# Kernel tuning notes

Hardware: AMD Instinct MI355X
Metric: run time of the kernel (lower is better)

## Reference

```python
import jax, jax.numpy as jnp
import numpy as np

D_MODEL = 1024
NUM_HEADS = 16
D_K = D_MODEL // NUM_HEADS
B, S = 2, 2048


def setup_inputs() -> dict:
    key = jax.random.key(0)
    ks = jax.random.split(key, 9)
    scale = 1.0 / np.sqrt(D_MODEL)
    return {
        "hidden_states": jax.random.normal(ks[0], (B, S, D_MODEL), dtype=jnp.float32),
        "attention_mask": jnp.ones((B, S, S), dtype=jnp.int32),
        "Wq": jax.random.normal(ks[1], (D_MODEL, D_MODEL), dtype=jnp.float32) * scale,
        "bq": jnp.zeros((D_MODEL,), dtype=jnp.float32),
        "Wk": jax.random.normal(ks[2], (D_MODEL, D_MODEL), dtype=jnp.float32) * scale,
        "bk": jnp.zeros((D_MODEL,), dtype=jnp.float32),
        "Wv": jax.random.normal(ks[3], (D_MODEL, D_MODEL), dtype=jnp.float32) * scale,
        "bv": jnp.zeros((D_MODEL,), dtype=jnp.float32),
        "Wo": jax.random.normal(ks[4], (D_MODEL, D_MODEL), dtype=jnp.float32) * scale,
        "bo": jnp.zeros((D_MODEL,), dtype=jnp.float32),
    }


def reference(hidden_states, attention_mask, Wq, bq, Wk, bk, Wv, bv, Wo, bo):
    b, s, _ = hidden_states.shape
    # torch Linear: y = x @ W.T + b
    def proj(W, bias):
        y = jnp.einsum('bsd,ed->bse', hidden_states, W) + bias
        return y.reshape(b, s, NUM_HEADS, D_K).transpose(0, 2, 1, 3)  # [B,H,S,dk]
    q = proj(Wq, bq)
    k = proj(Wk, bk)
    v = proj(Wv, bv)
    scores = jnp.einsum('bnqd,bnkd->bnqk', q, k) / np.sqrt(D_K)
    mask = attention_mask[:, None, :, :]  # [B,1,S,S]
    scores = jnp.where(mask == 0, jnp.float32(-1e9), scores)
    attn = jax.nn.softmax(scores, axis=-1)  # dropout = identity (eval)
    ctx = jnp.einsum('bnqk,bnkd->bnqd', attn, v)
    ctx = ctx.transpose(0, 2, 1, 3).reshape(b, s, D_MODEL)
    return jnp.einsum('bsd,ed->bse', ctx, Wo) + bo
```

## Files before the change

### kernel.cpp

```cpp
#include <hip/hip_runtime.h>

typedef short short8 __attribute__((ext_vector_type(8)));
typedef float floatx4 __attribute__((ext_vector_type(4)));
typedef float floatx16 __attribute__((ext_vector_type(16)));
typedef unsigned short ushort4v __attribute__((ext_vector_type(4)));

#define DEV static __device__ __forceinline__

DEV unsigned short f2bf(float f) {
  unsigned int u = __builtin_bit_cast(unsigned int, f);
  u += 0x7fffu + ((u >> 16) & 1u);
  return (unsigned short)(u >> 16);
}

DEV unsigned int cvtpk(float a, float b) {
  unsigned int r;
  asm("v_cvt_pk_bf16_f32 %0, %1, %2" : "=v"(r) : "v"(a), "v"(b));
  return r;
}

DEV void gload16(const unsigned short* g, unsigned short* l) {
  __builtin_amdgcn_global_load_lds((__attribute__((address_space(1))) void*)g,
                                   (__attribute__((address_space(3))) void*)l,
                                   16, 0, 0);
}

__global__ void convert_kernel(const float* __restrict__ hs, const float* __restrict__ Wq,
                               const float* __restrict__ Wk, const float* __restrict__ Wv,
                               const float* __restrict__ Wo,
                               unsigned short* __restrict__ xbf, unsigned short* __restrict__ wqkv,
                               unsigned short* __restrict__ wobf) {
  size_t i4 = ((size_t)blockIdx.x * 256 + threadIdx.x) * 4;
  const float* src;
  unsigned short* dst;
  if (i4 < 4194304) {
    src = hs + i4; dst = xbf + i4;
  } else if (i4 < 7340032) {
    size_t o = i4 - 4194304;
    size_t lo = o & 1048575;
    src = (o < 1048576) ? (Wq + lo) : ((o < 2097152) ? (Wk + lo) : (Wv + lo));
    dst = wqkv + o;
  } else {
    size_t o = i4 - 7340032;
    src = Wo + o; dst = wobf + o;
  }
  float4 v = *(const float4*)src;
  ushort4v u;
  u.x = f2bf(v.x); u.y = f2bf(v.y); u.z = f2bf(v.z); u.w = f2bf(v.w);
  *(ushort4v*)dst = u;
}

__global__ void maskpack_kernel(const int* __restrict__ mask, unsigned long long* __restrict__ bits) {
  int w = blockIdx.x * 256 + threadIdx.x;
  const int4* p = (const int4*)(mask + (size_t)w * 64);
  unsigned long long r = 0ull;
#pragma unroll
  for (int j = 0; j < 16; ++j) {
    int4 m = p[j];
    r |= (unsigned long long)(m.x != 0) << (j * 4 + 0);
    r |= (unsigned long long)(m.y != 0) << (j * 4 + 1);
    r |= (unsigned long long)(m.z != 0) << (j * 4 + 2);
    r |= (unsigned long long)(m.w != 0) << (j * 4 + 3);
  }
  bits[w] = r;
}

__global__ void __launch_bounds__(256) qkv_gemm(
    const unsigned short* __restrict__ X, const unsigned short* __restrict__ W,
    const float* __restrict__ bq, const float* __restrict__ bk, const float* __restrict__ bv,
    unsigned short* __restrict__ Qb, unsigned short* __restrict__ Kb,
    unsigned short* __restrict__ Vt) {
  __shared__ __align__(16) unsigned short As[128 * 32];
  __shared__ __align__(16) unsigned short Bs[128 * 32];
  const int tid = threadIdx.x;
  const int lane = tid & 63, wv = tid >> 6;
  const int wm = wv >> 1, wn = wv & 1;
  const int quad = lane >> 4, l15 = lane & 15;
  const int mb = blockIdx.y, nb = blockIdx.x;
  const bool sw = (nb < 16);

  const unsigned short* ga = X + (size_t)(mb * 128 + (tid >> 2)) * 1024 + (tid & 3) * 8;
  const unsigned short* gb = W + (size_t)(nb * 128 + (tid >> 2)) * 1024 + (tid & 3) * 8;
  unsigned short* la1 = As + tid * 8;
  unsigned short* la2 = As + 2048 + tid * 8;
  unsigned short* lb1 = Bs + tid * 8;
  unsigned short* lb2 = Bs + 2048 + tid * 8;

  const int wx = sw ? wn : wm;
  const int ww = sw ? wm : wn;

  floatx4 acc[4][4] = {};
  for (int kt = 0; kt < 32; ++kt) {
    const int k0 = kt * 32;
    gload16(ga + k0, la1);
    gload16(ga + k0 + 65536, la2);
    gload16(gb + k0, lb1);
    gload16(gb + k0 + 65536, lb2);
    __syncthreads();
    short8 xa[4], wb[4];
#pragma unroll
    for (int i = 0; i < 4; ++i) {
      xa[i] = *(const short8*)&As[(wx * 64 + i * 16 + l15) * 32 + quad * 8];
      wb[i] = *(const short8*)&Bs[(ww * 64 + i * 16 + l15) * 32 + quad * 8];
    }
    if (sw) {
#pragma unroll
      for (int mt = 0; mt < 4; ++mt)
#pragma unroll
        for (int nt = 0; nt < 4; ++nt)
          acc[mt][nt] = __builtin_amdgcn_mfma_f32_16x16x32_bf16(wb[mt], xa[nt], acc[mt][nt], 0, 0, 0);
    } else {
#pragma unroll
      for (int mt = 0; mt < 4; ++mt)
#pragma unroll
        for (int nt = 0; nt < 4; ++nt)
          acc[mt][nt] = __builtin_amdgcn_mfma_f32_16x16x32_bf16(xa[mt], wb[nt], acc[mt][nt], 0, 0, 0);
    }
    __syncthreads();
  }

  if (sw) {
#pragma unroll
    for (int mt = 0; mt < 4; ++mt) {
      const int wc0 = nb * 128 + wm * 64 + mt * 16 + quad * 4;
      const int mat = wc0 >> 10;
      const int nl0 = wc0 & 1023;
      const int hh = nl0 >> 6, d0 = nl0 & 63;
      const float4 b4 = *(const float4*)((mat ? bk : bq) + nl0);
      unsigned short* dst = mat ? Kb : Qb;
#pragma unroll
      for (int nt = 0; nt < 4; ++nt) {
        const int colx = mb * 128 + wn * 64 + nt * 16 + l15;
        const int bb = colx >> 11, s = colx & 2047;
        ushort4v pv;
        pv[0] = f2bf(acc[mt][nt][0] + b4.x);
        pv[1] = f2bf(acc[mt][nt][1] + b4.y);
        pv[2] = f2bf(acc[mt][nt][2] + b4.z);
        pv[3] = f2bf(acc[mt][nt][3] + b4.w);
        *(ushort4v*)&dst[((size_t)(bb * 16 + hh) * 2048 + s) * 64 + d0] = pv;
      }
    }
  } else {
#pragma unroll
    for (int nt = 0; nt < 4; ++nt) {
      const int col = nb * 128 + wn * 64 + nt * 16 + l15;
      const int nl = col & 1023;
      const float bias = bv[nl];
      const int hh = nl >> 6, d = nl & 63;
#pragma unroll
      for (int mt = 0; mt < 4; ++mt) {
        const int row0 = mb * 128 + wm * 64 + mt * 16 + quad * 4;
        const int bb = row0 >> 11, s = row0 & 2047;
        ushort4v pv;
#pragma unroll
        for (int r = 0; r < 4; ++r) pv[r] = f2bf(acc[mt][nt][r] + bias);
        *(ushort4v*)&Vt[((size_t)(bb * 16 + hh) * 64 + d) * 2048 + s] = pv;
      }
    }
  }
}

__global__ void __launch_bounds__(256, 4) attn_kernel(
    const unsigned short* __restrict__ Qb, const unsigned short* __restrict__ Kb,
    const unsigned short* __restrict__ Vt, const unsigned long long* __restrict__ mbits,
    unsigned short* __restrict__ ctx) {
  __shared__ __align__(16) unsigned short SM[4 * 64 * 64];
  const int tid = threadIdx.x;
  const int lane = tid & 63, wv = tid >> 6;
  const int l31 = lane & 31, h = lane >> 5;
  const int qg = wv & 1, h2 = wv >> 1;
  const int bid = (blockIdx.x & 7) * 128 + (blockIdx.x >> 3);
  const int pair = bid >> 5, qt = bid & 31;
  const int b_ = pair >> 4, hd = pair & 15;
  const int qrow = qt * 64 + qg * 32 + l31;
  const size_t pbase = (size_t)pair * (2048 * 64);
  const size_t vtb = (size_t)pair * (64 * 2048);

  short8 qf[4];
#pragma unroll
  for (int ks = 0; ks < 4; ++ks)
    qf[ks] = *(const short8*)(Qb + pbase + (size_t)qrow * 64 + ks * 16 + h * 8);

  unsigned short* Kh = SM + h2 * 4096;
  unsigned short* Vh = SM + 8192 + h2 * 4096;

  const int kLane = (lane >> 3) * 64 + (((lane & 7) ^ (lane >> 3)) * 8);
  const int vLane = (lane >> 3) * 2048 + (((lane & 7) ^ (lane >> 3)) * 8);
  const int cb = qg * 4;

  const unsigned long long* mrow = mbits + ((size_t)b_ * 2048 + qrow) * 32;

  floatx16 acc_o[2] = {};
  float lacc[2] = {0.f, 0.f};
  const float SCL = 0.125f * 1.44269504088896340736f;
  const float NC = -10.0f;

  for (int it = 0; it < 16; ++it) {
    const int tg = h2 * 16 + it;
    const unsigned short* kt = Kb + pbase + (size_t)tg * 4096;
    const unsigned short* vt = Vt + vtb + (size_t)tg * 64;
#pragma unroll
    for (int i = 0; i < 4; ++i) {
      gload16(kt + (cb + i) * 512 + kLane, Kh + (cb + i) * 512 + lane * 8);
      gload16(vt + (size_t)(cb + i) * 16384 + vLane, Vh + (cb + i) * 512 + lane * 8);
    }
    const unsigned long long w = mrow[tg];
    __syncthreads();

    floatx16 accs[2] = {};
    __builtin_amdgcn_s_setprio(1);
#pragma unroll
    for (int ks = 0; ks < 4; ++ks)
#pragma unroll
      for (int kb = 0; kb < 2; ++kb) {
        const int krow = kb * 32 + l31;
        short8 kf = *(const short8*)&Kh[krow * 64 + (((ks * 2 + h) ^ (krow & 7)) * 8)];
        accs[kb] = __builtin_amdgcn_mfma_f32_32x32x16_bf16(kf, qf[ks], accs[kb], 0, 0, 0);
      }
    __builtin_amdgcn_s_setprio(0);

    if (__any(w != ~0ull)) {
#pragma unroll
      for (int kb = 0; kb < 2; ++kb)
#pragma unroll
        for (int reg = 0; reg < 16; ++reg) {
          const int kl = (reg & 3) + 8 * (reg >> 2) + 4 * h;
          const int bit = kb * 32 + kl;
          if (!((w >> bit) & 1ull)) accs[kb][reg] = -6e9f;
        }
    }

#pragma unroll
    for (int kb = 0; kb < 2; ++kb) {
      unsigned int pk[8];
      float ls = 0.f;
#pragma unroll
      for (int i = 0; i < 8; ++i) {
        const float a = exp2f(fmaf(accs[kb][2 * i], SCL, NC));
        const float b = exp2f(fmaf(accs[kb][2 * i + 1], SCL, NC));
        ls += a + b;
        pk[i] = cvtpk(a, b);
      }
      lacc[kb] += ls;
#pragma unroll
      for (int u = 0; u < 2; ++u) {
        auto r02 = __builtin_amdgcn_permlane32_swap(pk[4 * u + 0], pk[4 * u + 2], false, false);
        auto r13 = __builtin_amdgcn_permlane32_swap(pk[4 * u + 1], pk[4 * u + 3], false, false);
        union { unsigned int w[4]; short8 s8; } af;
        af.w[0] = r02[0];
        af.w[1] = r13[0];
        af.w[2] = r02[1];
        af.w[3] = r13[1];
        const int t = kb * 2 + u;
        __builtin_amdgcn_s_setprio(1);
#pragma unroll
        for (int nt = 0; nt < 2; ++nt) {
          const int vrow = nt * 32 + l31;
          short8 vf = *(const short8*)&Vh[vrow * 64 + (((t * 2 + h) ^ (vrow & 7)) * 8)];
          acc_o[nt] = __builtin_amdgcn_mfma_f32_32x32x16_bf16(af.s8, vf, acc_o[nt], 0, 0, 0);
        }
        __builtin_amdgcn_s_setprio(0);
      }
    }
    __syncthreads();
  }

  float lsum = lacc[0] + lacc[1];
  lsum += __shfl_xor(lsum, 32);

  float* red = (float*)SM;
  if (h2 == 1) {
    float* p = red + (qg * 64 + lane) * 33;
#pragma unroll
    for (int reg = 0; reg < 16; ++reg) {
      p[reg] = acc_o[0][reg];
      p[16 + reg] = acc_o[1][reg];
    }
    p[32] = lsum;
  }
  __syncthreads();
  if (h2 == 0) {
    const float* p = red + (qg * 64 + lane) * 33;
#pragma unroll
    for (int reg = 0; reg < 16; ++reg) {
      acc_o[0][reg] += p[reg];
      acc_o[1][reg] += p[16 + reg];
    }
    lsum += p[32];
    const float rinv = 1.f / ((lsum > 0.f) ? lsum : 1.f);
#pragma unroll
    for (int reg = 0; reg < 16; ++reg) {
      const int ql = (reg & 3) + 8 * (reg >> 2) + 4 * h;
      const float rl = __shfl(rinv, ql);
      const size_t base = ((size_t)b_ * 2048 + qt * 64 + qg * 32 + ql) * 1024 + hd * 64;
      ctx[base + l31]      = f2bf(acc_o[0][reg] * rl);
      ctx[base + 32 + l31] = f2bf(acc_o[1][reg] * rl);
    }
  }
}

__global__ void __launch_bounds__(256) out_gemm(
    const unsigned short* __restrict__ C, const unsigned short* __restrict__ W,
    const float* __restrict__ bo, float* __restrict__ out) {
  __shared__ __align__(16) unsigned short As[128 * 32];
  __shared__ __align__(16) unsigned short Bs[128 * 32];
  const int tid = threadIdx.x;
  const int lane = tid & 63, wv = tid >> 6;
  const int wm = wv >> 1, wn = wv & 1;
  const int quad = lane >> 4, l15 = lane & 15;
  const int mb = blockIdx.y, nb = blockIdx.x;

  const unsigned short* ga = C + (size_t)(mb * 128 + (tid >> 2)) * 1024 + (tid & 3) * 8;
  const unsigned short* gb = W + (size_t)(nb * 128 + (tid >> 2)) * 1024 + (tid & 3) * 8;
  unsigned short* la1 = As + tid * 8;
  unsigned short* la2 = As + 2048 + tid * 8;
  unsigned short* lb1 = Bs + tid * 8;
  unsigned short* lb2 = Bs + 2048 + tid * 8;

  floatx4 acc[4][4] = {};
  for (int kt = 0; kt < 32; ++kt) {
    const int k0 = kt * 32;
    gload16(ga + k0, la1);
    gload16(ga + k0 + 65536, la2);
    gload16(gb + k0, lb1);
    gload16(gb + k0 + 65536, lb2);
    __syncthreads();
    short8 af[4], bfr[4];
#pragma unroll
    for (int i = 0; i < 4; ++i) {
      af[i]  = *(const short8*)&As[(wm * 64 + i * 16 + l15) * 32 + quad * 8];
      bfr[i] = *(const short8*)&Bs[(wn * 64 + i * 16 + l15) * 32 + quad * 8];
    }
#pragma unroll
    for (int mt = 0; mt < 4; ++mt)
#pragma unroll
      for (int nt = 0; nt < 4; ++nt)
        acc[mt][nt] = __builtin_amdgcn_mfma_f32_16x16x32_bf16(af[mt], bfr[nt], acc[mt][nt], 0, 0, 0);
    __syncthreads();
  }
#pragma unroll
  for (int nt = 0; nt < 4; ++nt) {
    const int col = nb * 128 + wn * 64 + nt * 16 + l15;
    const float bias = bo[col];
#pragma unroll
    for (int mt = 0; mt < 4; ++mt)
#pragma unroll
      for (int r = 0; r < 4; ++r) {
        const int row = mb * 128 + wm * 64 + mt * 16 + quad * 4 + r;
        out[(size_t)row * 1024 + col] = acc[mt][nt][r] + bias;
      }
  }
}

extern "C" void kernel_launch(void* const* d_in, const int* in_sizes, int n_in,
                              void* d_out, int out_size, void* d_ws, size_t ws_size,
                              hipStream_t stream) {
  const float* hs = (const float*)d_in[0];
  const int* mask = (const int*)d_in[1];
  const float* Wq = (const float*)d_in[2];
  const float* bq = (const float*)d_in[3];
  const float* Wk = (const float*)d_in[4];
  const float* bk = (const float*)d_in[5];
  const float* Wv = (const float*)d_in[6];
  const float* bv = (const float*)d_in[7];
  const float* Wo = (const float*)d_in[8];
  const float* bo = (const float*)d_in[9];
  float* out = (float*)d_out;

  char* ws = (char*)d_ws;
  unsigned short* xbf  = (unsigned short*)(ws + 0);
  unsigned short* wqkv = (unsigned short*)(ws + 8388608);
  unsigned short* wobf = (unsigned short*)(ws + 14680064);
  unsigned short* Qb   = (unsigned short*)(ws + 16777216);
  unsigned short* Kb   = (unsigned short*)(ws + 25165824);
  unsigned short* Vt   = (unsigned short*)(ws + 33554432);
  unsigned short* ctx  = (unsigned short*)(ws + 41943040);
  unsigned long long* mbits = (unsigned long long*)(ws + 50331648);

  convert_kernel<<<8192, 256, 0, stream>>>(hs, Wq, Wk, Wv, Wo, xbf, wqkv, wobf);
  maskpack_kernel<<<512, 256, 0, stream>>>(mask, mbits);
  qkv_gemm<<<dim3(24, 32), 256, 0, stream>>>(xbf, wqkv, bq, bk, bv, Qb, Kb, Vt);
  attn_kernel<<<1024, 256, 0, stream>>>(Qb, Kb, Vt, mbits, ctx);
  out_gemm<<<dim3(8, 32), 256, 0, stream>>>(ctx, wobf, bo, out);
}
```

Before: 267.1 us.

## Double-buffer K/V tiles and widen attention blocks to 128 query rows

The attention kernel now runs 512-thread blocks that each cover 128 query rows, so every K/V tile loaded into LDS is shared by twice as many query waves. LDS is split into two buffers, and the next tile's K/V and mask word are prefetched while the current tile is computed, so global load latency overlaps MFMA work. The score computation is also restructured per 32-key block to shorten live accumulator ranges. In exchange the block needs 64KB of LDS, which limits how many blocks fit per CU, and the grid shrinks to 512 blocks.

```diff
diff --git a/kernel.cpp b/kernel.cpp
--- a/kernel.cpp
+++ b/kernel.cpp
@@ -160,19 +160,21 @@
   }
 }
 
-__global__ void __launch_bounds__(256, 4) attn_kernel(
+__global__ __attribute__((amdgpu_flat_work_group_size(512, 512), amdgpu_waves_per_eu(4, 4)))
+void attn_kernel(
     const unsigned short* __restrict__ Qb, const unsigned short* __restrict__ Kb,
     const unsigned short* __restrict__ Vt, const unsigned long long* __restrict__ mbits,
     unsigned short* __restrict__ ctx) {
-  __shared__ __align__(16) unsigned short SM[4 * 64 * 64];
+  __shared__ __align__(16) unsigned short SM[2 * 4 * 4096];
   const int tid = threadIdx.x;
   const int lane = tid & 63, wv = tid >> 6;
   const int l31 = lane & 31, h = lane >> 5;
-  const int qg = wv & 1, h2 = wv >> 1;
-  const int bid = (blockIdx.x & 7) * 128 + (blockIdx.x >> 3);
-  const int pair = bid >> 5, qt = bid & 31;
+  const int qg = wv & 3, h2 = wv >> 2;
+  const int k2 = wv >> 1, sb = (wv & 1) * 4;
+  const int bid = (blockIdx.x & 7) * 64 + (blockIdx.x >> 3);
+  const int pair = bid >> 4, qt = bid & 15;
   const int b_ = pair >> 4, hd = pair & 15;
-  const int qrow = qt * 64 + qg * 32 + l31;
+  const int qrow = qt * 128 + qg * 32 + l31;
   const size_t pbase = (size_t)pair * (2048 * 64);
   const size_t vtb = (size_t)pair * (64 * 2048);
 
@@ -181,14 +183,25 @@
   for (int ks = 0; ks < 4; ++ks)
     qf[ks] = *(const short8*)(Qb + pbase + (size_t)qrow * 64 + ks * 16 + h * 8);
 
-  unsigned short* Kh = SM + h2 * 4096;
-  unsigned short* Vh = SM + 8192 + h2 * 4096;
-
   const int kLane = (lane >> 3) * 64 + (((lane & 7) ^ (lane >> 3)) * 8);
   const int vLane = (lane >> 3) * 2048 + (((lane & 7) ^ (lane >> 3)) * 8);
-  const int cb = qg * 4;
+  const unsigned short* kbase = Kb + pbase + (size_t)((k2 & 1) * 16) * 4096;
+  const unsigned short* vbase = Vt + vtb + (size_t)((k2 & 1) * 16) * 64;
+  unsigned short* ldst0 = SM + k2 * 4096 + sb * 512 + lane * 8;
 
   const unsigned long long* mrow = mbits + ((size_t)b_ * 2048 + qrow) * 32;
+
+  if (k2 < 2) {
+    const unsigned short* s = kbase + sb * 512 + kLane;
+#pragma unroll
+    for (int i = 0; i < 4; ++i) gload16(s + i * 512, ldst0 + i * 512);
+  } else {
+    const unsigned short* s = vbase + sb * 16384 + vLane;
+#pragma unroll
+    for (int i = 0; i < 4; ++i) gload16(s + i * 16384, ldst0 + i * 512);
+  }
+  unsigned long long w = mrow[h2 * 16];
+  __syncthreads();
 
   floatx16 acc_o[2] = {};
   float lacc[2] = {0.f, 0.f};
@@ -196,48 +209,49 @@
   const float NC = -10.0f;
 
   for (int it = 0; it < 16; ++it) {
-    const int tg = h2 * 16 + it;
-    const unsigned short* kt = Kb + pbase + (size_t)tg * 4096;
-    const unsigned short* vt = Vt + vtb + (size_t)tg * 64;
-#pragma unroll
-    for (int i = 0; i < 4; ++i) {
-      gload16(kt + (cb + i) * 512 + kLane, Kh + (cb + i) * 512 + lane * 8);
-      gload16(vt + (size_t)(cb + i) * 16384 + vLane, Vh + (cb + i) * 512 + lane * 8);
-    }
-    const unsigned long long w = mrow[tg];
-    __syncthreads();
-
-    floatx16 accs[2] = {};
-    __builtin_amdgcn_s_setprio(1);
-#pragma unroll
-    for (int ks = 0; ks < 4; ++ks)
-#pragma unroll
-      for (int kb = 0; kb < 2; ++kb) {
+    const int cur = it & 1;
+    const unsigned short* Kh = SM + cur * 16384 + h2 * 4096;
+    const unsigned short* Vh = SM + cur * 16384 + (2 + h2) * 4096;
+
+    if (it < 15) {
+      unsigned short* dst = ldst0 + (cur ^ 1) * 16384;
+      if (k2 < 2) {
+        const unsigned short* s = kbase + (size_t)(it + 1) * 4096 + sb * 512 + kLane;
+#pragma unroll
+        for (int i = 0; i < 4; ++i) gload16(s + i * 512, dst + i * 512);
+      } else {
+        const unsigned short* s = vbase + (size_t)(it + 1) * 64 + sb * 16384 + vLane;
+#pragma unroll
+        for (int i = 0; i < 4; ++i) gload16(s + i * 16384, dst + i * 512);
+      }
+    }
+    const unsigned long long nw = (it < 15) ? mrow[h2 * 16 + it + 1] : 0ull;
+    const bool needm = __any(w != ~0ull);
+
+#pragma unroll
+    for (int kb = 0; kb < 2; ++kb) {
+      floatx16 accs = {};
+      __builtin_amdgcn_s_setprio(1);
+#pragma unroll
+      for (int ks = 0; ks < 4; ++ks) {
         const int krow = kb * 32 + l31;
         short8 kf = *(const short8*)&Kh[krow * 64 + (((ks * 2 + h) ^ (krow & 7)) * 8)];
-        accs[kb] = __builtin_amdgcn_mfma_f32_32x32x16_bf16(kf, qf[ks], accs[kb], 0, 0, 0);
-      }
-    __builtin_amdgcn_s_setprio(0);
-
-    if (__any(w != ~0ull)) {
-#pragma unroll
-      for (int kb = 0; kb < 2; ++kb)
+        accs = __builtin_amdgcn_mfma_f32_32x32x16_bf16(kf, qf[ks], accs, 0, 0, 0);
+      }
+      __builtin_amdgcn_s_setprio(0);
+      if (needm) {
 #pragma unroll
         for (int reg = 0; reg < 16; ++reg) {
           const int kl = (reg & 3) + 8 * (reg >> 2) + 4 * h;
-          const int bit = kb * 32 + kl;
-          if (!((w >> bit) & 1ull)) accs[kb][reg] = -6e9f;
+          if (!((w >> (kb * 32 + kl)) & 1ull)) accs[reg] = -6e9f;
         }
-    }
-
-#pragma unroll
-    for (int kb = 0; kb < 2; ++kb) {
+      }
       unsigned int pk[8];
       float ls = 0.f;
 #pragma unroll
       for (int i = 0; i < 8; ++i) {
-        const float a = exp2f(fmaf(accs[kb][2 * i], SCL, NC));
-        const float b = exp2f(fmaf(accs[kb][2 * i + 1], SCL, NC));
+        const float a = exp2f(fmaf(accs[2 * i], SCL, NC));
+        const float b = exp2f(fmaf(accs[2 * i + 1], SCL, NC));
         ls += a + b;
         pk[i] = cvtpk(a, b);
       }
@@ -246,11 +260,11 @@
       for (int u = 0; u < 2; ++u) {
         auto r02 = __builtin_amdgcn_permlane32_swap(pk[4 * u + 0], pk[4 * u + 2], false, false);
         auto r13 = __builtin_amdgcn_permlane32_swap(pk[4 * u + 1], pk[4 * u + 3], false, false);
-        union { unsigned int w[4]; short8 s8; } af;
-        af.w[0] = r02[0];
-        af.w[1] = r13[0];
-        af.w[2] = r02[1];
-        af.w[3] = r13[1];
+        union { unsigned int wd[4]; short8 s8; } af;
+        af.wd[0] = r02[0];
+        af.wd[1] = r13[0];
+        af.wd[2] = r02[1];
+        af.wd[3] = r13[1];
         const int t = kb * 2 + u;
         __builtin_amdgcn_s_setprio(1);
 #pragma unroll
@@ -263,6 +277,7 @@
       }
     }
     __syncthreads();
+    w = nw;
   }
 
   float lsum = lacc[0] + lacc[1];
@@ -292,7 +307,7 @@
     for (int reg = 0; reg < 16; ++reg) {
       const int ql = (reg & 3) + 8 * (reg >> 2) + 4 * h;
       const float rl = __shfl(rinv, ql);
-      const size_t base = ((size_t)b_ * 2048 + qt * 64 + qg * 32 + ql) * 1024 + hd * 64;
+      const size_t base = ((size_t)b_ * 2048 + qt * 128 + qg * 32 + ql) * 1024 + hd * 64;
       ctx[base + l31]      = f2bf(acc_o[0][reg] * rl);
       ctx[base + 32 + l31] = f2bf(acc_o[1][reg] * rl);
     }
@@ -380,6 +395,6 @@
   convert_kernel<<<8192, 256, 0, stream>>>(hs, Wq, Wk, Wv, Wo, xbf, wqkv, wobf);
   maskpack_kernel<<<512, 256, 0, stream>>>(mask, mbits);
   qkv_gemm<<<dim3(24, 32), 256, 0, stream>>>(xbf, wqkv, bq, bk, bv, Qb, Kb, Vt);
-  attn_kernel<<<1024, 256, 0, stream>>>(Qb, Kb, Vt, mbits, ctx);
+  attn_kernel<<<512, 512, 0, stream>>>(Qb, Kb, Vt, mbits, ctx);
   out_gemm<<<dim3(8, 32), 256, 0, stream>>>(ctx, wobf, bo, out);
 }
```

Result: no change. 268.5 us (+0.5%).
